# Performance work log

Measured on AMD Instinct MI355X. Metric: run time of the kernel, lower is better.

Reference implementation:

```python
import jax, jax.numpy as jnp
import numpy as np

SEQ_LEN, BATCH, HID, ATT = 2048, 64, 512, 512


def setup_inputs() -> dict:
    key = jax.random.key(0)
    k1, k2, k3, k4, k5, k6 = jax.random.split(key, 6)
    return {
        "dec_out": jax.random.normal(k1, (BATCH, HID), dtype=jnp.float32),
        "enc_outs": jax.random.normal(k2, (SEQ_LEN, BATCH, HID), dtype=jnp.float32),
        "W_s": jax.random.normal(k3, (ATT, HID), dtype=jnp.float32) * (1.0 / np.sqrt(HID)),
        "W_t": jax.random.normal(k4, (ATT, HID), dtype=jnp.float32) * (1.0 / np.sqrt(HID)),
        "b_t": jax.random.normal(k5, (ATT,), dtype=jnp.float32) * 0.01,
        "v_a": jax.random.uniform(k6, (ATT,), dtype=jnp.float32, minval=-0.05, maxval=0.05),
    }


def reference(dec_out, enc_outs, W_s, W_t, b_t, v_a):
    # enc_att: (seq_len, batch, att) = W_s @ enc_outs
    enc_att = jnp.einsum('sbh,ah->sba', enc_outs, W_s)
    # dec_att: (batch, att) = W_t @ dec_out + b_t
    dec_att = dec_out @ W_t.T + b_t
    # score(b, s) = v_a . tanh(enc_att[s,b] + dec_att[b])
    scores = jnp.einsum('sba,a->bs', jnp.tanh(enc_att + dec_att[None, :, :]), v_a)
    return scores  # (batch, seq_len)
```

## Files before the change

### kernel.cpp

```cpp
#include <hip/hip_runtime.h>

typedef __attribute__((ext_vector_type(8))) short short8;
typedef __attribute__((ext_vector_type(4))) float f32x4;

#define SEQ 2048
#define BATCH 64
#define HID 512
#define ATT 512

__device__ __forceinline__ unsigned short f2bf(float f) {
  unsigned u = __float_as_uint(f);
  u += 0x7fffu + ((u >> 16) & 1u);
  return (unsigned short)(u >> 16);
}

__device__ __forceinline__ void dma16(const void* g, void* l) {
  __builtin_amdgcn_global_load_lds(
      (const __attribute__((address_space(1))) unsigned int*)g,
      (__attribute__((address_space(3))) unsigned int*)l, 16, 0, 0);
}

__device__ __forceinline__ short8 cvt8(float4 lo, float4 hi) {
  union { unsigned u[4]; short8 s; } r;
  asm("v_cvt_pk_bf16_f32 %0, %1, %2" : "=v"(r.u[0]) : "v"(lo.x), "v"(lo.y));
  asm("v_cvt_pk_bf16_f32 %0, %1, %2" : "=v"(r.u[1]) : "v"(lo.z), "v"(lo.w));
  asm("v_cvt_pk_bf16_f32 %0, %1, %2" : "=v"(r.u[2]) : "v"(hi.x), "v"(hi.y));
  asm("v_cvt_pk_bf16_f32 %0, %1, %2" : "=v"(r.u[3]) : "v"(hi.z), "v"(hi.w));
  return r.s;
}

#define GLOADS(dst, voff, base, OFF) \
  asm volatile("global_load_dwordx4 %0, %1, %2 offset:" #OFF \
               : "=v"(dst) : "v"(voff), "s"(base))

#define BWAIT(N, b0, b1, b2, b3) \
  asm volatile("s_waitcnt vmcnt(" #N ")" \
               : "+v"(b0), "+v"(b1), "+v"(b2), "+v"(b3) :: "memory")

#define DSREAD(dst, vaddr, IMM) \
  asm volatile("ds_read_b128 %0, %1 offset:%2" \
               : "=v"(dst) : "v"(vaddr), "i"(IMM))

__global__ void bahdanau_pre(const float* __restrict__ dec_out,
                             const float* __restrict__ W_t,
                             const float* __restrict__ b_t,
                             const float* __restrict__ W_s,
                             unsigned short* __restrict__ wsb,
                             float* __restrict__ decT) {
  if (blockIdx.x < 64) {
    const int b = blockIdx.x;
    __shared__ float drow[HID];
    for (int i = threadIdx.x; i < HID; i += 256) drow[i] = dec_out[b * HID + i];
    __syncthreads();
    for (int a = threadIdx.x; a < ATT; a += 256) {
      const float4* wr = (const float4*)(W_t + (size_t)a * HID);
      float s0 = 0.f, s1 = 0.f, s2 = 0.f, s3 = 0.f;
#pragma unroll 4
      for (int j = 0; j < HID / 4; ++j) {
        float4 w = wr[j];
        s0 = fmaf(w.x, drow[4 * j + 0], s0);
        s1 = fmaf(w.y, drow[4 * j + 1], s1);
        s2 = fmaf(w.z, drow[4 * j + 2], s2);
        s3 = fmaf(w.w, drow[4 * j + 3], s3);
      }
      decT[a * BATCH + b] = (s0 + s1) + (s2 + s3) + b_t[a];
    }
  } else {
    const int cb = blockIdx.x - 64;
    const float4* src = (const float4*)W_s;
#pragma unroll
    for (int i = 0; i < 4; ++i) {
      int idx = cb * 1024 + i * 256 + threadIdx.x;
      float4 v = src[idx];
      int a = idx >> 7;
      int h = (idx & 127) * 4;
      ushort4 o;
      o.x = f2bf(v.x); o.y = f2bf(v.y); o.z = f2bf(v.z); o.w = f2bf(v.w);
      int blk = (a >> 4) * 64 + ((h >> 3) & 3) * 16 + (a & 15);
      int dst = (h >> 5) * 16384 + blk * 8 + (h & 7);
      *(ushort4*)&wsb[dst] = o;
    }
  }
}

__global__ __launch_bounds__(512, 2)
void bahdanau_main(const float* __restrict__ enc,
                   const unsigned short* __restrict__ wsb,
                   const float* __restrict__ decT,
                   const float* __restrict__ v_a,
                   float* __restrict__ out) {
  __shared__ __align__(16) float Asm[8][2048];
  __shared__ float partial[512];

  const int tid  = threadIdx.x;
  const int w    = tid >> 6;
  const int lane = tid & 63;
  const int c = lane & 15;
  const int q = lane >> 4;
  const int x7 = c & 7;
  const int s = blockIdx.x;
  const int n0 = w * 64;

  const char* encB = (const char*)(enc + (size_t)s * 64 * HID);

  const int am   = w * 8 + (lane >> 3);
  const int jsrc = (lane & 7) ^ (lane >> 3);
  const char* aSrc = encB + am * 2048 + jsrc * 16;

  const unsigned voff = (unsigned)(w * 256 + q * 16 + c) * 16u;

  const unsigned lA = (unsigned)(size_t)(__attribute__((address_space(3))) char*)&Asm[0][0];
  const unsigned loOff = lA + (unsigned)(c * 128 + (((2 * q)    ) ^ x7) * 16);
  const unsigned hiOff = lA + (unsigned)(c * 128 + (((2 * q) | 1) ^ x7) * 16);

  f32x4 acc[4][4];
#pragma unroll
  for (int nt = 0; nt < 4; ++nt)
#pragma unroll
    for (int mt = 0; mt < 4; ++mt)
      acc[mt][nt] = *(const f32x4*)(decT + (size_t)(n0 + nt * 16 + c) * 64 + mt * 16 + q * 4);

  asm volatile("s_waitcnt vmcnt(0)" ::: "memory");

  short8 bf[2][4];

  dma16(aSrc,       (char*)&Asm[0][0] + w * 1024);
  dma16(aSrc + 128, (char*)&Asm[1][0] + w * 1024);
  dma16(aSrc + 256, (char*)&Asm[2][0] + w * 1024);
  dma16(aSrc + 384, (char*)&Asm[3][0] + w * 1024);
  GLOADS(bf[0][0], voff, wsb, 0);
  GLOADS(bf[0][1], voff, wsb, 1024);
  GLOADS(bf[0][2], voff, wsb, 2048);
  GLOADS(bf[0][3], voff, wsb, 3072);

#pragma unroll
  for (int kb = 0; kb < 16; ++kb) {
    if (kb + 1 < 16) {
      const unsigned short* bk = wsb + (size_t)(kb + 1) * 16384;
      GLOADS(bf[(kb + 1) & 1][0], voff, bk, 0);
      GLOADS(bf[(kb + 1) & 1][1], voff, bk, 1024);
      GLOADS(bf[(kb + 1) & 1][2], voff, bk, 2048);
      GLOADS(bf[(kb + 1) & 1][3], voff, bk, 3072);
    }
    if (kb + 4 < 16)
      dma16(aSrc + (kb + 4) * 128, (char*)&Asm[(kb + 4) & 7][0] + w * 1024);

    if (kb == 0)       BWAIT(5, bf[kb & 1][0], bf[kb & 1][1], bf[kb & 1][2], bf[kb & 1][3]);
    else if (kb <= 11) BWAIT(6, bf[kb & 1][0], bf[kb & 1][1], bf[kb & 1][2], bf[kb & 1][3]);
    else if (kb == 12) BWAIT(5, bf[kb & 1][0], bf[kb & 1][1], bf[kb & 1][2], bf[kb & 1][3]);
    else if (kb <= 14) BWAIT(4, bf[kb & 1][0], bf[kb & 1][1], bf[kb & 1][2], bf[kb & 1][3]);
    else               BWAIT(0, bf[kb & 1][0], bf[kb & 1][1], bf[kb & 1][2], bf[kb & 1][3]);
    __builtin_amdgcn_s_barrier();

    float4 lo0, hi0, lo1, hi1, lo2, hi2, lo3, hi3;
    DSREAD(lo0, loOff, ((kb & 7) * 8192 + 0 * 2048));
    DSREAD(hi0, hiOff, ((kb & 7) * 8192 + 0 * 2048));
    DSREAD(lo1, loOff, ((kb & 7) * 8192 + 1 * 2048));
    DSREAD(hi1, hiOff, ((kb & 7) * 8192 + 1 * 2048));
    DSREAD(lo2, loOff, ((kb & 7) * 8192 + 2 * 2048));
    DSREAD(hi2, hiOff, ((kb & 7) * 8192 + 2 * 2048));
    DSREAD(lo3, loOff, ((kb & 7) * 8192 + 3 * 2048));
    DSREAD(hi3, hiOff, ((kb & 7) * 8192 + 3 * 2048));
    asm volatile("s_waitcnt lgkmcnt(0)" ::: "memory");
    __builtin_amdgcn_sched_barrier(0);

    short8 af0 = cvt8(lo0, hi0);
    short8 af1 = cvt8(lo1, hi1);
    short8 af2 = cvt8(lo2, hi2);
    short8 af3 = cvt8(lo3, hi3);
#pragma unroll
    for (int nt = 0; nt < 4; ++nt) {
      acc[0][nt] = __builtin_amdgcn_mfma_f32_16x16x32_bf16(af0, bf[kb & 1][nt], acc[0][nt], 0, 0, 0);
      acc[1][nt] = __builtin_amdgcn_mfma_f32_16x16x32_bf16(af1, bf[kb & 1][nt], acc[1][nt], 0, 0, 0);
      acc[2][nt] = __builtin_amdgcn_mfma_f32_16x16x32_bf16(af2, bf[kb & 1][nt], acc[2][nt], 0, 0, 0);
      acc[3][nt] = __builtin_amdgcn_mfma_f32_16x16x32_bf16(af3, bf[kb & 1][nt], acc[3][nt], 0, 0, 0);
    }
  }

  float va[4];
#pragma unroll
  for (int nt = 0; nt < 4; ++nt) va[nt] = v_a[n0 + nt * 16 + c];

  float rowsum[4][4];
#pragma unroll
  for (int mt = 0; mt < 4; ++mt) {
#pragma unroll
    for (int r = 0; r < 4; ++r) {
      float sum = 0.f;
#pragma unroll
      for (int nt = 0; nt < 4; ++nt) {
        float x = acc[mt][nt][r];
        float e = __builtin_amdgcn_exp2f(x * 2.8853900817779268f);
        float t = 1.f - 2.f * __builtin_amdgcn_rcpf(e + 1.f);
        sum = fmaf(va[nt], t, sum);
      }
      rowsum[mt][r] = sum;
    }
  }

#pragma unroll
  for (int off = 1; off < 16; off <<= 1) {
#pragma unroll
    for (int mt = 0; mt < 4; ++mt)
#pragma unroll
      for (int r = 0; r < 4; ++r)
        rowsum[mt][r] += __shfl_xor(rowsum[mt][r], off, 64);
  }

  if (c == 0) {
#pragma unroll
    for (int mt = 0; mt < 4; ++mt)
#pragma unroll
      for (int r = 0; r < 4; ++r)
        partial[w * 64 + mt * 16 + q * 4 + r] = rowsum[mt][r];
  }
  __syncthreads();

  if (tid < 64) {
    float sum = 0.f;
#pragma unroll
    for (int ww = 0; ww < 8; ++ww) sum += partial[ww * 64 + tid];
    out[(size_t)tid * SEQ + s] = sum;
  }
}

extern "C" void kernel_launch(void* const* d_in, const int* in_sizes, int n_in,
                              void* d_out, int out_size, void* d_ws, size_t ws_size,
                              hipStream_t stream) {
  const float* dec_out = (const float*)d_in[0];
  const float* enc     = (const float*)d_in[1];
  const float* W_s     = (const float*)d_in[2];
  const float* W_t     = (const float*)d_in[3];
  const float* b_t     = (const float*)d_in[4];
  const float* v_a     = (const float*)d_in[5];
  float* out = (float*)d_out;

  unsigned short* wsb = (unsigned short*)d_ws;
  float* decT = (float*)((char*)d_ws + (size_t)ATT * HID * 2);

  bahdanau_pre<<<128, 256, 0, stream>>>(dec_out, W_t, b_t, W_s, wsb, decT);
  bahdanau_main<<<SEQ, 512, 0, stream>>>(enc, wsb, decT, v_a, out);
}
```

Measured before the change: 469.1 us.

## Split attention dimension across two 256-thread blocks with atomic score accumulation

Each sequence position is now handled by two blocks of 4 waves, each covering half of the attention dimension, and their partial scores are combined with atomicAdd into an output zeroed by the pre-kernel. The LDS A staging becomes a 3-deep ring of two k-slices per stage, and each block starts its k loop at a staggered offset based on the sequence index, likely to spread reads of the shared weight tiles. The aim is more resident blocks per CU and better latency hiding. In exchange the encoder tile is read twice, and the change adds float atomics and a dependence on the zeroing done by the pre-kernel.

```diff
diff --git a/kernel.cpp b/kernel.cpp
--- a/kernel.cpp
+++ b/kernel.cpp
@@ -46,7 +46,10 @@
                              const float* __restrict__ b_t,
                              const float* __restrict__ W_s,
                              unsigned short* __restrict__ wsb,
-                             float* __restrict__ decT) {
+                             float* __restrict__ decT,
+                             float* __restrict__ out) {
+  ((float4*)out)[blockIdx.x * 256 + threadIdx.x] = make_float4(0.f, 0.f, 0.f, 0.f);
+
   if (blockIdx.x < 64) {
     const int b = blockIdx.x;
     __shared__ float drow[HID];
@@ -83,14 +86,14 @@
   }
 }
 
-__global__ __launch_bounds__(512, 2)
+__global__ __launch_bounds__(256, 3)
 void bahdanau_main(const float* __restrict__ enc,
                    const unsigned short* __restrict__ wsb,
                    const float* __restrict__ decT,
                    const float* __restrict__ v_a,
                    float* __restrict__ out) {
-  __shared__ __align__(16) float Asm[8][2048];
-  __shared__ float partial[512];
+  __shared__ __align__(16) float Abuf[3][2][2048];
+  __shared__ float partial[256];
 
   const int tid  = threadIdx.x;
   const int w    = tid >> 6;
@@ -98,18 +101,21 @@
   const int c = lane & 15;
   const int q = lane >> 4;
   const int x7 = c & 7;
-  const int s = blockIdx.x;
-  const int n0 = w * 64;
+  const int bid = blockIdx.x;
+  const int s = bid >> 1;
+  const int h = bid & 1;
+  const int n0 = h * 256 + w * 64;
+  const int t0 = (s & 7) * 2;
 
   const char* encB = (const char*)(enc + (size_t)s * 64 * HID);
 
-  const int am   = w * 8 + (lane >> 3);
+  const int am   = w * 16 + (lane >> 3);
   const int jsrc = (lane & 7) ^ (lane >> 3);
   const char* aSrc = encB + am * 2048 + jsrc * 16;
 
-  const unsigned voff = (unsigned)(w * 256 + q * 16 + c) * 16u;
-
-  const unsigned lA = (unsigned)(size_t)(__attribute__((address_space(3))) char*)&Asm[0][0];
+  const unsigned voff = (unsigned)(((h * 4 + w) * 256 + q * 16 + c) * 16);
+
+  const unsigned lA = (unsigned)(size_t)(__attribute__((address_space(3))) char*)&Abuf[0][0][0];
   const unsigned loOff = lA + (unsigned)(c * 128 + (((2 * q)    ) ^ x7) * 16);
   const unsigned hiOff = lA + (unsigned)(c * 128 + (((2 * q) | 1) ^ x7) * 16);
 
@@ -124,43 +130,49 @@
 
   short8 bf[2][4];
 
-  dma16(aSrc,       (char*)&Asm[0][0] + w * 1024);
-  dma16(aSrc + 128, (char*)&Asm[1][0] + w * 1024);
-  dma16(aSrc + 256, (char*)&Asm[2][0] + w * 1024);
-  dma16(aSrc + 384, (char*)&Asm[3][0] + w * 1024);
-  GLOADS(bf[0][0], voff, wsb, 0);
-  GLOADS(bf[0][1], voff, wsb, 1024);
-  GLOADS(bf[0][2], voff, wsb, 2048);
-  GLOADS(bf[0][3], voff, wsb, 3072);
-
-#pragma unroll
-  for (int kb = 0; kb < 16; ++kb) {
-    if (kb + 1 < 16) {
-      const unsigned short* bk = wsb + (size_t)(kb + 1) * 16384;
-      GLOADS(bf[(kb + 1) & 1][0], voff, bk, 0);
-      GLOADS(bf[(kb + 1) & 1][1], voff, bk, 1024);
-      GLOADS(bf[(kb + 1) & 1][2], voff, bk, 2048);
-      GLOADS(bf[(kb + 1) & 1][3], voff, bk, 3072);
-    }
-    if (kb + 4 < 16)
-      dma16(aSrc + (kb + 4) * 128, (char*)&Asm[(kb + 4) & 7][0] + w * 1024);
-
-    if (kb == 0)       BWAIT(5, bf[kb & 1][0], bf[kb & 1][1], bf[kb & 1][2], bf[kb & 1][3]);
-    else if (kb <= 11) BWAIT(6, bf[kb & 1][0], bf[kb & 1][1], bf[kb & 1][2], bf[kb & 1][3]);
-    else if (kb == 12) BWAIT(5, bf[kb & 1][0], bf[kb & 1][1], bf[kb & 1][2], bf[kb & 1][3]);
-    else if (kb <= 14) BWAIT(4, bf[kb & 1][0], bf[kb & 1][1], bf[kb & 1][2], bf[kb & 1][3]);
-    else               BWAIT(0, bf[kb & 1][0], bf[kb & 1][1], bf[kb & 1][2], bf[kb & 1][3]);
-    __builtin_amdgcn_s_barrier();
+#define STAGE(a, b) do { \
+    const char* s_ = aSrc + (size_t)(((t0 + 2 * (a)) & 15) * 128); \
+    char* d_ = (char*)&Abuf[(b)][0][0] + w * 2048; \
+    dma16(s_,                d_); \
+    dma16(s_ + 16384,        d_ + 1024); \
+    dma16(s_ + 128,          d_ + 8192); \
+    dma16(s_ + 128 + 16384,  d_ + 8192 + 1024); \
+  } while (0)
+
+#define LOADB(set, t_) do { \
+    const unsigned short* bk_ = wsb + (size_t)(t_) * 16384; \
+    GLOADS(bf[set][0], voff, bk_, 0); \
+    GLOADS(bf[set][1], voff, bk_, 1024); \
+    GLOADS(bf[set][2], voff, bk_, 2048); \
+    GLOADS(bf[set][3], voff, bk_, 3072); \
+  } while (0)
+
+  STAGE(0, 0);
+  STAGE(1, 1);
+  LOADB(0, t0);
+  asm volatile("s_waitcnt vmcnt(8)" ::: "memory");
+  __builtin_amdgcn_s_barrier();
+
+#pragma unroll
+  for (int i = 0; i < 16; ++i) {
+    const int g = i >> 1, j = i & 1, buf = (i >> 1) % 3;
+
+    if (i + 1 < 16) LOADB((i + 1) & 1, (t0 + i + 1) & 15);
+    if (j == 0 && g + 2 <= 7) STAGE(g + 2, (g + 2) % 3);
+
+    if (i <= 11)      BWAIT(8, bf[i & 1][0], bf[i & 1][1], bf[i & 1][2], bf[i & 1][3]);
+    else if (i <= 14) BWAIT(4, bf[i & 1][0], bf[i & 1][1], bf[i & 1][2], bf[i & 1][3]);
+    else              BWAIT(0, bf[i & 1][0], bf[i & 1][1], bf[i & 1][2], bf[i & 1][3]);
 
     float4 lo0, hi0, lo1, hi1, lo2, hi2, lo3, hi3;
-    DSREAD(lo0, loOff, ((kb & 7) * 8192 + 0 * 2048));
-    DSREAD(hi0, hiOff, ((kb & 7) * 8192 + 0 * 2048));
-    DSREAD(lo1, loOff, ((kb & 7) * 8192 + 1 * 2048));
-    DSREAD(hi1, hiOff, ((kb & 7) * 8192 + 1 * 2048));
-    DSREAD(lo2, loOff, ((kb & 7) * 8192 + 2 * 2048));
-    DSREAD(hi2, hiOff, ((kb & 7) * 8192 + 2 * 2048));
-    DSREAD(lo3, loOff, ((kb & 7) * 8192 + 3 * 2048));
-    DSREAD(hi3, hiOff, ((kb & 7) * 8192 + 3 * 2048));
+    DSREAD(lo0, loOff, (buf * 16384 + j * 8192 + 0 * 2048));
+    DSREAD(hi0, hiOff, (buf * 16384 + j * 8192 + 0 * 2048));
+    DSREAD(lo1, loOff, (buf * 16384 + j * 8192 + 1 * 2048));
+    DSREAD(hi1, hiOff, (buf * 16384 + j * 8192 + 1 * 2048));
+    DSREAD(lo2, loOff, (buf * 16384 + j * 8192 + 2 * 2048));
+    DSREAD(hi2, hiOff, (buf * 16384 + j * 8192 + 2 * 2048));
+    DSREAD(lo3, loOff, (buf * 16384 + j * 8192 + 3 * 2048));
+    DSREAD(hi3, hiOff, (buf * 16384 + j * 8192 + 3 * 2048));
     asm volatile("s_waitcnt lgkmcnt(0)" ::: "memory");
     __builtin_amdgcn_sched_barrier(0);
 
@@ -170,12 +182,16 @@
     short8 af3 = cvt8(lo3, hi3);
 #pragma unroll
     for (int nt = 0; nt < 4; ++nt) {
-      acc[0][nt] = __builtin_amdgcn_mfma_f32_16x16x32_bf16(af0, bf[kb & 1][nt], acc[0][nt], 0, 0, 0);
-      acc[1][nt] = __builtin_amdgcn_mfma_f32_16x16x32_bf16(af1, bf[kb & 1][nt], acc[1][nt], 0, 0, 0);
-      acc[2][nt] = __builtin_amdgcn_mfma_f32_16x16x32_bf16(af2, bf[kb & 1][nt], acc[2][nt], 0, 0, 0);
-      acc[3][nt] = __builtin_amdgcn_mfma_f32_16x16x32_bf16(af3, bf[kb & 1][nt], acc[3][nt], 0, 0, 0);
-    }
-  }
+      acc[0][nt] = __builtin_amdgcn_mfma_f32_16x16x32_bf16(af0, bf[i & 1][nt], acc[0][nt], 0, 0, 0);
+      acc[1][nt] = __builtin_amdgcn_mfma_f32_16x16x32_bf16(af1, bf[i & 1][nt], acc[1][nt], 0, 0, 0);
+      acc[2][nt] = __builtin_amdgcn_mfma_f32_16x16x32_bf16(af2, bf[i & 1][nt], acc[2][nt], 0, 0, 0);
+      acc[3][nt] = __builtin_amdgcn_mfma_f32_16x16x32_bf16(af3, bf[i & 1][nt], acc[3][nt], 0, 0, 0);
+    }
+
+    if (j == 1 && g < 7) __builtin_amdgcn_s_barrier();
+  }
+#undef STAGE
+#undef LOADB
 
   float va[4];
 #pragma unroll
@@ -219,8 +235,8 @@
   if (tid < 64) {
     float sum = 0.f;
 #pragma unroll
-    for (int ww = 0; ww < 8; ++ww) sum += partial[ww * 64 + tid];
-    out[(size_t)tid * SEQ + s] = sum;
+    for (int ww = 0; ww < 4; ++ww) sum += partial[ww * 64 + tid];
+    atomicAdd(&out[(size_t)tid * SEQ + s], sum);
   }
 }
 
@@ -238,6 +254,6 @@
   unsigned short* wsb = (unsigned short*)d_ws;
   float* decT = (float*)((char*)d_ws + (size_t)ATT * HID * 2);
 
-  bahdanau_pre<<<128, 256, 0, stream>>>(dec_out, W_t, b_t, W_s, wsb, decT);
-  bahdanau_main<<<SEQ, 512, 0, stream>>>(enc, wsb, decT, v_a, out);
-}
+  bahdanau_pre<<<128, 256, 0, stream>>>(dec_out, W_t, b_t, W_s, wsb, decT, out);
+  bahdanau_main<<<SEQ * 2, 256, 0, stream>>>(enc, wsb, decT, v_a, out);
+}
```

Measured after the change: 459.5 us. 2.0% less time.
